# Optimization experiments

Measured on AMD Instinct MI355X. Metric: run time of the kernel, lower is better.

Reference implementation:

```python
import math
import jax, jax.numpy as jnp
import numpy as np

V = 50257
D = 1024
K_HOT = 1024
R_HOT = 768
HID = 1024
N_FREQS = 48


def setup_inputs() -> dict:
    key = jax.random.key(0)
    ks = jax.random.split(key, 10)
    tokens = jax.random.randint(ks[0], (2, 1024), 0, V, dtype=jnp.int32)
    # default hot_ids = arange(K) -> both permutations are identity
    old_to_new = jnp.arange(V, dtype=jnp.int32)
    new_to_old = jnp.arange(V, dtype=jnp.int32)
    freqs = (2.0 ** jnp.linspace(0.0, math.log2(V), N_FREQS)).astype(jnp.float32)
    in_dim = 2 * N_FREQS + 8  # 104
    U = jax.random.normal(ks[1], (K_HOT, R_HOT), jnp.float32) / math.sqrt(R_HOT)
    B = jax.random.normal(ks[2], (R_HOT, D), jnp.float32) / math.sqrt(R_HOT)
    W1 = jax.random.normal(ks[3], (in_dim, HID), jnp.float32) / math.sqrt(in_dim)
    b1 = jnp.zeros((HID,), jnp.float32)
    W2 = jax.random.normal(ks[4], (HID, HID), jnp.float32) / math.sqrt(HID)
    b2 = jnp.zeros((HID,), jnp.float32)
    W3 = jax.random.normal(ks[5], (HID, D), jnp.float32) * 0.02
    b3 = jnp.zeros((D,), jnp.float32)
    tail_gain = jnp.asarray(1.0, jnp.float32)
    log_alpha = jnp.asarray(0.0, jnp.float32)
    out_bias = jnp.zeros((V,), jnp.float32)
    return dict(tokens=tokens, old_to_new=old_to_new, new_to_old=new_to_old,
                freqs=freqs, U=U, B=B, W1=W1, b1=b1, W2=W2, b2=b2, W3=W3, b3=b3,
                tail_gain=tail_gain, log_alpha=log_alpha, out_bias=out_bias)


def _fourier(ids, freqs):
    # ids: int[...] -> features [..., 2*n_freqs + 8]
    x = ids.astype(jnp.float32) / float(V)
    theta = x[..., None] * freqs  # [..., n_freqs]
    bits = jnp.stack([((ids >> (2 * k)) & 3).astype(jnp.float32) / 3.0
                      for k in range(8)], axis=-1)
    return jnp.concatenate([jnp.sin(theta), jnp.cos(theta), bits], axis=-1)


def _hyper(phi, W1, b1, W2, b2, W3, b3):
    h = jax.nn.gelu(phi @ W1 + b1, approximate=False)
    h = jax.nn.gelu(h @ W2 + b2, approximate=False)
    return h @ W3 + b3


def reference(tokens, old_to_new, new_to_old, freqs, U, B, W1, b1, W2, b2, W3, b3,
              tail_gain, log_alpha, out_bias):
    # ---- encode ----
    new_tok = old_to_new[tokens]                       # [B,S]
    is_hot = new_tok < K_HOT
    hot_rows = U[jnp.clip(new_tok, 0, K_HOT - 1)] @ B  # [B,S,d]
    phi = _fourier(tokens, freqs)
    cold_rows = _hyper(phi, W1, b1, W2, b2, W3, b3) * tail_gain
    latent = jnp.where(is_hot[..., None], hot_rows, cold_rows)  # [B,S,d]
    # ---- decode ----
    hot_all = U @ B                                    # [K,d]
    cold_orig = new_to_old[K_HOT:]
    phi_cold = _fourier(cold_orig, freqs)
    cold_all = _hyper(phi_cold, W1, b1, W2, b2, W3, b3) * tail_gain  # [V-K,d]
    E = jnp.concatenate([hot_all, cold_all], axis=0)   # [V,d] new-id order
    logits_new = latent @ E.T                          # [B,S,V]
    logits = jnp.take(logits_new, old_to_new, axis=-1) # reorder to original ids
    return logits * jnp.exp(log_alpha) + out_bias
```

## Files before the change

### kernel.cpp

```cpp
#include <hip/hip_runtime.h>
#include <stdint.h>

typedef unsigned short u16;
typedef __attribute__((ext_vector_type(8))) short short8;
typedef __attribute__((ext_vector_type(4))) float f32x4;

#define VOCAB 50257
#define KHOT  1024

__device__ __forceinline__ float bf2f(u16 u) {
  union { uint32_t i; float f; } c; c.i = ((uint32_t)u) << 16; return c.f;
}
__device__ __forceinline__ u16 f2bf(float f) {
  union { float f; uint32_t i; } c; c.f = f;
  uint32_t r = (c.i + 0x7FFFu + ((c.i >> 16) & 1u)) >> 16;
  return (u16)r;
}
__device__ __forceinline__ float ldf(const void* p, size_t i, int f32) {
  return f32 ? ((const float*)p)[i] : bf2f(((const u16*)p)[i]);
}

#define GLOAD16(gp, lp)                                                        \
  __builtin_amdgcn_global_load_lds(                                            \
      (const __attribute__((address_space(1))) void*)(gp),                     \
      (__attribute__((address_space(3))) void*)(lp), 16, 0, 0)

__global__ void detect_kernel(const void* __restrict__ freqs, int* __restrict__ flags) {
  uint32_t w = *(const uint32_t*)freqs;
  flags[0] = ((w & 0xFFFFu) == 0u) ? 1 : 0;
}

__global__ void normalize_bf16(const void* __restrict__ src, u16* __restrict__ dst,
                               int n, const int* __restrict__ flags) {
  int f32 = flags[0];
  int i = blockIdx.x * 256 + threadIdx.x;
  if (i < n) dst[i] = f2bf(ldf(src, i, f32));
}

__global__ void phi_kernel(const int* __restrict__ tok, int c0,
                           const void* __restrict__ freqs, u16* __restrict__ PHI,
                           const int* __restrict__ flags) {
  int f32 = flags[0];
  int row = blockIdx.x;
  int t = threadIdx.x;
  int id = tok ? tok[row] : (c0 + row);
  float x = (float)id / (float)VOCAB;
  float v = 0.0f;
  if (t < 48)       v = sinf(x * ldf(freqs, t, f32));
  else if (t < 96)  v = cosf(x * ldf(freqs, t - 48, f32));
  else if (t < 104) v = (float)((id >> (2 * (t - 96))) & 3) * (1.0f / 3.0f);
  PHI[(size_t)row * 128 + t] = f2bf(v);
}

__global__ void transpose_pad(const void* __restrict__ src, u16* __restrict__ dst,
                              int Ksrc, int N, int Kpad, const int* __restrict__ flags) {
  int f32 = flags[0];
  __shared__ u16 tile[32][33];
  int kb = blockIdx.x * 32, nb = blockIdx.y * 32;
  int tx = threadIdx.x & 31, ty = threadIdx.x >> 5;
  for (int i = ty; i < 32; i += 8) {
    int k = kb + i, n = nb + tx;
    u16 v = 0;
    if (k < Ksrc && n < N) v = f2bf(ldf(src, (size_t)k * N + n, f32));
    tile[i][tx] = v;
  }
  __syncthreads();
  for (int i = ty; i < 32; i += 8) {
    int n = nb + i, k = kb + tx;
    if (n < N && k < Kpad) dst[(size_t)n * Kpad + k] = tile[tx][i];
  }
}

__global__ void overwrite_hot(u16* __restrict__ E, const int* __restrict__ tok, int c0,
                              const int* __restrict__ o2n, const u16* __restrict__ Hot) {
  int row = blockIdx.x;
  int id;
  if (tok) id = tok[row];
  else { id = c0 + row; if (id >= VOCAB) return; }
  int k = o2n[id];
  if (k < KHOT) {
    int t = threadIdx.x;
    *(uint4*)(E + (size_t)row * 1024 + t * 8) =
        *(const uint4*)(Hot + (size_t)k * 1024 + t * 8);
  }
}

#define BM 128
#define BN 128
#define BK 64
__global__ __launch_bounds__(256) void gemm_bt(
    const u16* __restrict__ A, const u16* __restrict__ Bt, void* __restrict__ C,
    int M, int N, int K, int ldc, int col_off, int n_limit,
    const void* __restrict__ bias,
    const void* __restrict__ scale_ptr, int scale_mode, int op,
    const int* __restrict__ flags, int c_is_out) {
  __shared__ __attribute__((aligned(16))) u16 As[2][BM * BK];
  __shared__ __attribute__((aligned(16))) u16 Bs[2][BN * BK];
  const int tid  = threadIdx.x;
  const int lane = tid & 63;
  const int wave = tid >> 6;
  const int wr = wave >> 1, wc = wave & 1;

  const int gx = gridDim.x;
  const int nwg = gx * gridDim.y;
  const int orig = blockIdx.y * gx + blockIdx.x;
  const int xcd = orig & 7, local = orig >> 3;
  const int q = nwg >> 3, r = nwg & 7;
  const int w = (xcd < r ? xcd * (q + 1) : r * (q + 1) + (xcd - r) * q) + local;
  const int m0 = (w % gx) * BM;
  const int n0 = (w / gx) * BN;
  const int f32 = flags[0];

  f32x4 acc[4][4];
#pragma unroll
  for (int i = 0; i < 4; ++i)
#pragma unroll
    for (int j = 0; j < 4; ++j) acc[i][j] = (f32x4){0.f, 0.f, 0.f, 0.f};

  const int srow = tid >> 3;
  const int skb  = (tid & 7) ^ (srow & 7);
  const size_t sgoff = (size_t)srow * K + skb * 8;
  const int wbase = tid & 192;

  const int nsteps = K / BK;

#pragma unroll
  for (int p = 0; p < 4; ++p) {
    GLOAD16(A  + (size_t)(m0 + p * 32) * K + sgoff, &As[0][(p * 256 + wbase) * 8]);
    GLOAD16(Bt + (size_t)(n0 + p * 32) * K + sgoff, &Bs[0][(p * 256 + wbase) * 8]);
  }

  for (int s = 0; s < nsteps; ++s) {
    const int cur = s & 1;
    __syncthreads();
    if (s + 1 < nsteps) {
      const size_t kt = (size_t)(s + 1) * BK;
#pragma unroll
      for (int p = 0; p < 4; ++p) {
        GLOAD16(A  + (size_t)(m0 + p * 32) * K + kt + sgoff, &As[cur ^ 1][(p * 256 + wbase) * 8]);
        GLOAD16(Bt + (size_t)(n0 + p * 32) * K + kt + sgoff, &Bs[cur ^ 1][(p * 256 + wbase) * 8]);
      }
    }
#pragma unroll
    for (int ks = 0; ks < 2; ++ks) {
      short8 af[4], bfr[4];
#pragma unroll
      for (int t = 0; t < 4; ++t) {
        int m  = wr * 64 + t * 16 + (lane & 15);
        int kb = ks * 4 + (lane >> 4);
        int sw = kb ^ (lane & 7);
        af[t]  = *(const short8*)(&As[cur][m * BK + sw * 8]);
        int n  = wc * 64 + t * 16 + (lane & 15);
        bfr[t] = *(const short8*)(&Bs[cur][n * BK + sw * 8]);
      }
#pragma unroll
      for (int i = 0; i < 4; ++i)
#pragma unroll
        for (int j = 0; j < 4; ++j)
          acc[i][j] = __builtin_amdgcn_mfma_f32_16x16x32_bf16(af[i], bfr[j], acc[i][j], 0, 0, 0);
    }
  }

  float s = 1.0f;
  if (scale_ptr) {
    float sv = ldf(scale_ptr, 0, f32);
    s = (scale_mode == 2) ? expf(sv) : sv;
  }
  const int store_f32 = c_is_out && f32;
#pragma unroll
  for (int i = 0; i < 4; ++i) {
#pragma unroll
    for (int j = 0; j < 4; ++j) {
      int n = n0 + wc * 64 + j * 16 + (lane & 15);
      if (n < n_limit) {
        float bv = bias ? ldf(bias, (size_t)col_off + n, f32) : 0.0f;
#pragma unroll
        for (int r2 = 0; r2 < 4; ++r2) {
          int m = m0 + wr * 64 + i * 16 + ((lane >> 4) << 2) + r2;
          float v = acc[i][j][r2];
          float outv;
          if (op == 0)      outv = s * (v + bv);
          else if (op == 1) { float x = v + bv; outv = 0.5f * x * (1.0f + erff(x * 0.70710678118654752f)); }
          else              outv = s * v + bv;
          size_t cidx = (size_t)m * ldc + col_off + n;
          if (store_f32) ((float*)C)[cidx] = outv;
          else           ((u16*)C)[cidx]   = f2bf(outv);
        }
      }
    }
  }
}

static inline size_t alignup(size_t x) { return (x + 255) & ~(size_t)255; }

extern "C" void kernel_launch(void* const* d_in, const int* in_sizes, int n_in,
                              void* d_out, int out_size, void* d_ws, size_t ws_size,
                              hipStream_t stream) {
  const int* tokens     = (const int*)d_in[0];
  const int* o2n        = (const int*)d_in[1];
  const void* freqs     = d_in[3];
  const void* U         = d_in[4];
  const void* Bm        = d_in[5];
  const void* W1        = d_in[6];
  const void* b1        = d_in[7];
  const void* W2        = d_in[8];
  const void* b2        = d_in[9];
  const void* W3        = d_in[10];
  const void* b3        = d_in[11];
  const void* tail_gain = d_in[12];
  const void* log_alpha = d_in[13];
  const void* out_bias  = d_in[14];
  const int T = in_sizes[0];

  char* ws = (char*)d_ws;
  size_t off = 0;
  auto take = [&](size_t bytes) { char* p = ws + off; off += alignup(bytes); return p; };
  int* flags = (int*)take(256);
  u16* W1t = (u16*)take((size_t)1024 * 128 * 2);
  u16* W2t = (u16*)take((size_t)1024 * 1024 * 2);
  u16* W3t = (u16*)take((size_t)1024 * 1024 * 2);
  u16* Btr = (u16*)take((size_t)1024 * 768 * 2);
  u16* Un  = (u16*)take((size_t)1024 * 768 * 2);
  u16* Hot = (u16*)take((size_t)1024 * 1024 * 2);
  u16* Lat = (u16*)take((size_t)T * 1024 * 2);
  size_t fixed = off;
  int chunk = 2048;
  {
    size_t avail = (ws_size > fixed + 4096) ? (ws_size - fixed - 4096) : 0;
    long maxrows = (long)(avail / 4352);
    long c = (maxrows / 128) * 128;
    if (c > 50432) c = 50432;
    if (c < 2048)  c = 2048;
    if (c < T)     c = T;
    chunk = (int)c;
  }
  u16* PHI = (u16*)take((size_t)chunk * 128 * 2);
  u16* H1  = (u16*)take((size_t)chunk * 1024 * 2);
  u16* H2  = (u16*)take((size_t)chunk * 1024 * 2);

  detect_kernel<<<1, 1, 0, stream>>>(freqs, flags);

  transpose_pad<<<dim3(4, 32),  256, 0, stream>>>(W1, W1t, 104, 1024, 128, flags);
  transpose_pad<<<dim3(32, 32), 256, 0, stream>>>(W2, W2t, 1024, 1024, 1024, flags);
  transpose_pad<<<dim3(32, 32), 256, 0, stream>>>(W3, W3t, 1024, 1024, 1024, flags);
  transpose_pad<<<dim3(24, 32), 256, 0, stream>>>(Bm, Btr, 768, 1024, 768, flags);
  normalize_bf16<<<(1024 * 768 + 255) / 256, 256, 0, stream>>>(U, Un, 1024 * 768, flags);

  gemm_bt<<<dim3(8, 8), 256, 0, stream>>>(Un, Btr, Hot, 1024, 1024, 768, 1024, 0, 1024,
                                          nullptr, nullptr, 0, 0, flags, 0);

  phi_kernel<<<T, 128, 0, stream>>>(tokens, 0, freqs, PHI, flags);
  gemm_bt<<<dim3(T / 128, 8), 256, 0, stream>>>(PHI, W1t, H2, T, 1024, 128, 1024, 0, 1024,
                                                b1, nullptr, 0, 1, flags, 0);
  gemm_bt<<<dim3(T / 128, 8), 256, 0, stream>>>(H2, W2t, H1, T, 1024, 1024, 1024, 0, 1024,
                                                b2, nullptr, 0, 1, flags, 0);
  gemm_bt<<<dim3(T / 128, 8), 256, 0, stream>>>(H1, W3t, Lat, T, 1024, 1024, 1024, 0, 1024,
                                                b3, tail_gain, 1, 0, flags, 0);
  overwrite_hot<<<T, 128, 0, stream>>>(Lat, tokens, 0, o2n, Hot);

  for (int c0 = 0; c0 < VOCAB; c0 += chunk) {
    int rows = VOCAB - c0;
    int Mc = rows >= chunk ? chunk : ((rows + 127) / 128) * 128;
    phi_kernel<<<Mc, 128, 0, stream>>>(nullptr, c0, freqs, PHI, flags);
    gemm_bt<<<dim3(Mc / 128, 8), 256, 0, stream>>>(PHI, W1t, H2, Mc, 1024, 128, 1024, 0, 1024,
                                                   b1, nullptr, 0, 1, flags, 0);
    gemm_bt<<<dim3(Mc / 128, 8), 256, 0, stream>>>(H2, W2t, H1, Mc, 1024, 1024, 1024, 0, 1024,
                                                   b2, nullptr, 0, 1, flags, 0);
    gemm_bt<<<dim3(Mc / 128, 8), 256, 0, stream>>>(H1, W3t, H2, Mc, 1024, 1024, 1024, 0, 1024,
                                                   b3, tail_gain, 1, 0, flags, 0);
    u16* Echunk = H2;
    overwrite_hot<<<Mc, 128, 0, stream>>>(Echunk, nullptr, c0, o2n, Hot);
    int nlim = rows < Mc ? rows : Mc;
    gemm_bt<<<dim3(T / 128, Mc / 128), 256, 0, stream>>>(Lat, Echunk, d_out, T, Mc, 1024,
                                                         VOCAB, c0, nlim, out_bias,
                                                         log_alpha, 2, 2, flags, 1);
  }
  (void)n_in; (void)out_size; (void)in_sizes;
}
```

Before: 1.613 ms.

## Add 256x256-tile GEMM with XCD-aware block remap for large vocab GEMMs

```diff
diff --git a/kernel.cpp b/kernel.cpp
--- a/kernel.cpp
+++ b/kernel.cpp
@@ -83,6 +83,12 @@
     *(uint4*)(E + (size_t)row * 1024 + t * 8) =
         *(const uint4*)(Hot + (size_t)k * 1024 + t * 8);
   }
+}
+
+__device__ __forceinline__ float epi_op(float v, float bv, float s, int op) {
+  if (op == 0) return s * (v + bv);
+  if (op == 1) { float x = v + bv; return 0.5f * x * (1.0f + erff(x * 0.70710678118654752f)); }
+  return s * v + bv;
 }
 
 #define BM 128
@@ -177,11 +183,110 @@
 #pragma unroll
         for (int r2 = 0; r2 < 4; ++r2) {
           int m = m0 + wr * 64 + i * 16 + ((lane >> 4) << 2) + r2;
-          float v = acc[i][j][r2];
-          float outv;
-          if (op == 0)      outv = s * (v + bv);
-          else if (op == 1) { float x = v + bv; outv = 0.5f * x * (1.0f + erff(x * 0.70710678118654752f)); }
-          else              outv = s * v + bv;
+          float outv = epi_op(acc[i][j][r2], bv, s, op);
+          size_t cidx = (size_t)m * ldc + col_off + n;
+          if (store_f32) ((float*)C)[cidx] = outv;
+          else           ((u16*)C)[cidx]   = f2bf(outv);
+        }
+      }
+    }
+  }
+}
+
+#define CM 256
+#define CN 256
+__global__ __launch_bounds__(512, 2) void gemm256_bt(
+    const u16* __restrict__ A, const u16* __restrict__ Bt, void* __restrict__ C,
+    int M, int N, int K, int ldc, int col_off, int n_limit,
+    const void* __restrict__ bias,
+    const void* __restrict__ scale_ptr, int scale_mode, int op,
+    const int* __restrict__ flags, int c_is_out) {
+  __shared__ __attribute__((aligned(16))) u16 As[2][CM * BK];
+  __shared__ __attribute__((aligned(16))) u16 Bs[2][CN * BK];
+  const int tid  = threadIdx.x;
+  const int lane = tid & 63;
+  const int wave = tid >> 6;
+  const int wr = wave >> 2;
+  const int wc = wave & 3;
+
+  const int gx = gridDim.x;
+  const int nwg = gx * gridDim.y;
+  const int orig = blockIdx.y * gx + blockIdx.x;
+  const int xcd = orig & 7, local = orig >> 3;
+  const int q = nwg >> 3, r = nwg & 7;
+  const int w = (xcd < r ? xcd * (q + 1) : r * (q + 1) + (xcd - r) * q) + local;
+  const int m0 = (w % gx) * CM;
+  const int n0 = (w / gx) * CN;
+  const int f32 = flags[0];
+
+  f32x4 acc[8][4];
+#pragma unroll
+  for (int i = 0; i < 8; ++i)
+#pragma unroll
+    for (int j = 0; j < 4; ++j) acc[i][j] = (f32x4){0.f, 0.f, 0.f, 0.f};
+
+  const int srow = tid >> 3;
+  const int skb  = (tid & 7) ^ (srow & 7);
+  const size_t sgoff = (size_t)srow * K + skb * 8;
+  const int wbase = tid & 448;
+
+  const int nsteps = K / BK;
+
+#pragma unroll
+  for (int p = 0; p < 4; ++p) {
+    GLOAD16(A  + (size_t)(m0 + p * 64) * K + sgoff, &As[0][(p * 512 + wbase) * 8]);
+    GLOAD16(Bt + (size_t)(n0 + p * 64) * K + sgoff, &Bs[0][(p * 512 + wbase) * 8]);
+  }
+
+  for (int s = 0; s < nsteps; ++s) {
+    const int cur = s & 1;
+    __syncthreads();
+    if (s + 1 < nsteps) {
+      const size_t kt = (size_t)(s + 1) * BK;
+#pragma unroll
+      for (int p = 0; p < 4; ++p) {
+        GLOAD16(A  + (size_t)(m0 + p * 64) * K + kt + sgoff, &As[cur ^ 1][(p * 512 + wbase) * 8]);
+        GLOAD16(Bt + (size_t)(n0 + p * 64) * K + kt + sgoff, &Bs[cur ^ 1][(p * 512 + wbase) * 8]);
+      }
+    }
+#pragma unroll
+    for (int ks = 0; ks < 2; ++ks) {
+      const int kb = ks * 4 + (lane >> 4);
+      const int sw = kb ^ (lane & 7);
+      short8 bfr[4];
+#pragma unroll
+      for (int j = 0; j < 4; ++j) {
+        int n = wc * 64 + j * 16 + (lane & 15);
+        bfr[j] = *(const short8*)(&Bs[cur][n * BK + sw * 8]);
+      }
+#pragma unroll
+      for (int i = 0; i < 8; ++i) {
+        int m = wr * 128 + i * 16 + (lane & 15);
+        short8 af = *(const short8*)(&As[cur][m * BK + sw * 8]);
+#pragma unroll
+        for (int j = 0; j < 4; ++j)
+          acc[i][j] = __builtin_amdgcn_mfma_f32_16x16x32_bf16(af, bfr[j], acc[i][j], 0, 0, 0);
+      }
+    }
+  }
+
+  float s = 1.0f;
+  if (scale_ptr) {
+    float sv = ldf(scale_ptr, 0, f32);
+    s = (scale_mode == 2) ? expf(sv) : sv;
+  }
+  const int store_f32 = c_is_out && f32;
+#pragma unroll
+  for (int i = 0; i < 8; ++i) {
+#pragma unroll
+    for (int j = 0; j < 4; ++j) {
+      int n = n0 + wc * 64 + j * 16 + (lane & 15);
+      if (n < n_limit) {
+        float bv = bias ? ldf(bias, (size_t)col_off + n, f32) : 0.0f;
+#pragma unroll
+        for (int r2 = 0; r2 < 4; ++r2) {
+          int m = m0 + wr * 128 + i * 16 + ((lane >> 4) << 2) + r2;
+          float outv = epi_op(acc[i][j][r2], bv, s, op);
           size_t cidx = (size_t)m * ldc + col_off + n;
           if (store_f32) ((float*)C)[cidx] = outv;
           else           ((u16*)C)[cidx]   = f2bf(outv);
@@ -228,7 +333,7 @@
   {
     size_t avail = (ws_size > fixed + 4096) ? (ws_size - fixed - 4096) : 0;
     long maxrows = (long)(avail / 4352);
-    long c = (maxrows / 128) * 128;
+    long c = (maxrows / 256) * 256;
     if (c > 50432) c = 50432;
     if (c < 2048)  c = 2048;
     if (c < T)     c = T;
@@ -260,20 +365,20 @@
 
   for (int c0 = 0; c0 < VOCAB; c0 += chunk) {
     int rows = VOCAB - c0;
-    int Mc = rows >= chunk ? chunk : ((rows + 127) / 128) * 128;
+    int Mc = rows >= chunk ? chunk : ((rows + 255) / 256) * 256;
     phi_kernel<<<Mc, 128, 0, stream>>>(nullptr, c0, freqs, PHI, flags);
     gemm_bt<<<dim3(Mc / 128, 8), 256, 0, stream>>>(PHI, W1t, H2, Mc, 1024, 128, 1024, 0, 1024,
                                                    b1, nullptr, 0, 1, flags, 0);
-    gemm_bt<<<dim3(Mc / 128, 8), 256, 0, stream>>>(H2, W2t, H1, Mc, 1024, 1024, 1024, 0, 1024,
-                                                   b2, nullptr, 0, 1, flags, 0);
-    gemm_bt<<<dim3(Mc / 128, 8), 256, 0, stream>>>(H1, W3t, H2, Mc, 1024, 1024, 1024, 0, 1024,
-                                                   b3, tail_gain, 1, 0, flags, 0);
+    gemm256_bt<<<dim3(Mc / 256, 4), 512, 0, stream>>>(H2, W2t, H1, Mc, 1024, 1024, 1024, 0, 1024,
+                                                      b2, nullptr, 0, 1, flags, 0);
+    gemm256_bt<<<dim3(Mc / 256, 4), 512, 0, stream>>>(H1, W3t, H2, Mc, 1024, 1024, 1024, 0, 1024,
+                                                      b3, tail_gain, 1, 0, flags, 0);
     u16* Echunk = H2;
     overwrite_hot<<<Mc, 128, 0, stream>>>(Echunk, nullptr, c0, o2n, Hot);
     int nlim = rows < Mc ? rows : Mc;
-    gemm_bt<<<dim3(T / 128, Mc / 128), 256, 0, stream>>>(Lat, Echunk, d_out, T, Mc, 1024,
-                                                         VOCAB, c0, nlim, out_bias,
-                                                         log_alpha, 2, 2, flags, 1);
+    gemm256_bt<<<dim3(T / 256, Mc / 256), 512, 0, stream>>>(Lat, Echunk, d_out, T, Mc, 1024,
+                                                            VOCAB, c0, nlim, out_bias,
+                                                            log_alpha, 2, 2, flags, 1);
   }
   (void)n_in; (void)out_size; (void)in_sizes;
 }
```

Result: slower. 1.660 ms (+2.9%).
